# Kernel tuning notes

Measured on AMD Instinct MI355X. Metric: run time of the kernel, lower is better.

Reference implementation:

```python
import jax, jax.numpy as jnp
import numpy as np

N_NODES = 100000
N_EDGES = 1600000
D_IN = 64
D_OUT = 64
BN_EPS = 1e-5


def setup_inputs() -> dict:
    key = jax.random.key(0)
    ks = jax.random.split(key, 8)
    x = jax.random.normal(ks[0], (N_NODES, D_IN), dtype=jnp.float32)
    edge_index = jax.random.randint(ks[1], (2, N_EDGES), 0, N_NODES, dtype=jnp.int64)
    s_e = 1.0 / np.sqrt(2 * D_IN)
    s_n = 1.0 / np.sqrt(D_IN + D_OUT)
    W_edge = jax.random.uniform(ks[2], (2 * D_IN, D_OUT), jnp.float32, -s_e, s_e)
    b_edge = jax.random.uniform(ks[3], (D_OUT,), jnp.float32, -s_e, s_e)
    W_node = jax.random.uniform(ks[4], (D_IN + D_OUT, D_OUT), jnp.float32, -s_n, s_n)
    b_node = jax.random.uniform(ks[5], (D_OUT,), jnp.float32, -s_n, s_n)
    prelu_a = jnp.asarray(0.25, dtype=jnp.float32)  # nn.PReLU default single slope
    bn_gamma = jnp.ones((D_OUT,), dtype=jnp.float32)
    bn_beta = jnp.zeros((D_OUT,), dtype=jnp.float32)
    return {"x": x, "edge_index": edge_index, "W_edge": W_edge, "b_edge": b_edge,
            "W_node": W_node, "b_node": b_node, "prelu_a": prelu_a,
            "bn_gamma": bn_gamma, "bn_beta": bn_beta}


def reference(x, edge_index, W_edge, b_edge, W_node, b_node, prelu_a, bn_gamma, bn_beta):
    src, dst = edge_index[0], edge_index[1]
    # edge model: message from concat(source, target) node features  [E, 2*D_IN]
    msg_in = jnp.concatenate([x[src], x[dst]], axis=-1)
    msg = msg_in @ W_edge + b_edge                              # [E, D_OUT]
    # scatter-sum aggregate messages at destination nodes       [N, D_OUT]
    agg = jax.ops.segment_sum(msg, dst, num_segments=N_NODES)
    # node model
    h = jnp.concatenate([x, agg], axis=-1) @ W_node + b_node    # [N, D_OUT]
    # PReLU (single shared slope)
    h = jnp.where(h >= 0, h, prelu_a * h)
    # BatchNorm over nodes (training-mode batch stats, biased variance)
    mean = jnp.mean(h, axis=0)
    var = jnp.mean(jnp.square(h - mean), axis=0)
    h = (h - mean) * jax.lax.rsqrt(var + BN_EPS) * bn_gamma + bn_beta
    return h
```

## Files before the change

kernel.cpp:

```cpp
#include <hip/hip_runtime.h>
#include <hip/hip_fp16.h>

typedef _Float16 f16x8 __attribute__((ext_vector_type(8)));
typedef _Float16 f16x4 __attribute__((ext_vector_type(4)));
typedef float f32x4 __attribute__((ext_vector_type(4)));
typedef float f32x2 __attribute__((ext_vector_type(2)));

#define NPB 256
#define FCHUNK 6144
#define MAXBK 512
#define SEGCAP 64
#define CAP8 6144

__global__ __launch_bounds__(1024) void k_prepfill(
    const float4* __restrict__ x4, __half2* __restrict__ xh2,
    unsigned* __restrict__ xq, int n4, int X2,
    const int* __restrict__ src, const int* __restrict__ dst,
    int* __restrict__ cnt, int* __restrict__ packed2, int E, int FGRID,
    const float* __restrict__ We, const float* __restrict__ be,
    const float* __restrict__ Wn, __half* __restrict__ Wfrag, float* __restrict__ c2,
    float* __restrict__ stats, int nbuck, int N) {
  int b = blockIdx.x, t = threadIdx.x;
  if (b < X2) {
    int i = b * 1024 + t;
    if (i < n4) {
      float4 v = x4[i];
      __half2 a, c;
      a.x = __float2half_rn(v.x); a.y = __float2half_rn(v.y);
      c.x = __float2half_rn(v.z); c.y = __float2half_rn(v.w);
      xh2[2 * i] = a;
      xh2[2 * i + 1] = c;
      int w = __builtin_amdgcn_cvt_pk_fp8_f32(v.x, v.y, 0, false);
      w = __builtin_amdgcn_cvt_pk_fp8_f32(v.z, v.w, w, true);
      xq[i] = (unsigned)w;
    }
  } else if (b < X2 + 24) {
    int mb = b - X2;
    if (t < 512) {
      int mat = mb >> 3, kk = (mb >> 2) & 1, ct = mb & 3;
      int lane = t >> 3, j = t & 7;
      int k = kk * 32 + ((lane >> 4) & 3) * 8 + j;
      int col = ct * 16 + (lane & 15);
      float v;
      if (mat == 0) {
        v = Wn[k * 64 + col];
      } else if (mat == 1) {
        float a = 0.f;
        for (int m = 0; m < 64; ++m) a += We[k * 64 + m] * Wn[(64 + m) * 64 + col];
        v = a;
      } else {
        float a = 0.f;
        for (int m = 0; m < 64; ++m) a += We[(64 + k) * 64 + m] * Wn[(64 + m) * 64 + col];
        v = a;
      }
      Wfrag[mb * 512 + t] = __float2half_rn(v);
    }
  } else if (b == X2 + 24) {
    if (t < 64) {
      float a = 0.f;
      for (int m = 0; m < 64; ++m) a += be[m] * Wn[(64 + m) * 64 + t];
      c2[t] = a;
    } else if (t < 96) {
      __half2 z; z.x = __float2half_rn(0.f); z.y = __float2half_rn(0.f);
      xh2[(size_t)N * 32 + (t - 64)] = z;
    } else if (t < 112) {
      xq[(size_t)N * 16 + (t - 96)] = 0u;
    } else if (t >= 128 && t < 256) {
      stats[t - 128] = 0.f;
    }
  } else {
    int fb = b - (X2 + 25);
    __shared__ int lh[MAXBK];
    int e0 = fb * FCHUNK;
    int e1 = min(e0 + FCHUNK, E);
    for (int i = t; i < MAXBK; i += 1024) lh[i] = 0;
    __syncthreads();
    int dv[6];
#pragma unroll
    for (int i = 0; i < 6; ++i) {
      int e = e0 + t + i * 1024;
      dv[i] = (e < e1) ? dst[e] : -1;
      if (dv[i] >= 0) atomicAdd(&lh[dv[i] >> 8], 1);
    }
    __syncthreads();
    for (int i = t; i < MAXBK; i += 1024) {
      if (i < nbuck) cnt[(size_t)i * FGRID + fb] = lh[i];
      lh[i] = 0;
    }
    __syncthreads();
#pragma unroll
    for (int i = 0; i < 6; ++i) {
      int d = dv[i];
      if (d >= 0) {
        int e = e0 + t + i * 1024;
        int bk = d >> 8;
        unsigned lp = (unsigned)atomicAdd(&lh[bk], 1);
        if (lp < SEGCAP)
          packed2[((size_t)bk * FGRID + fb) * SEGCAP + lp] = src[e] | ((d & 255) << 20);
      }
    }
  }
}

__global__ __launch_bounds__(1024) void k_sort(const int* __restrict__ packed2,
    const int* __restrict__ cnt, int* __restrict__ csr,
    int* __restrict__ offA, int* __restrict__ deg, int FGRID, int N) {
  __shared__ int scnt[288];
  __shared__ int hist[NPB];
  __shared__ int sc[NPB];
  __shared__ int curs[NPB];
  int b = blockIdx.x, t = threadIdx.x;
  if (t < NPB) hist[t] = 0;
  for (int i = t; i < FGRID; i += 1024) scnt[i] = cnt[(size_t)b * FGRID + i];
  __syncthreads();
  int slots = FGRID * SEGCAP;
  const int* seg = packed2 + (size_t)b * FGRID * SEGCAP;
  for (int idx = t; idx < slots; idx += 1024) {
    int s = idx >> 6, k = idx & 63;
    if (k < scnt[s]) atomicAdd(&hist[(seg[idx] >> 20) & 255], 1);
  }
  __syncthreads();
  int v = (t < NPB) ? hist[t] : 0;
  int pv = (v + 7) & ~7;
  if (t < NPB) sc[t] = pv;
  __syncthreads();
  for (int d = 1; d < 256; d <<= 1) {
    int a = (t >= d && t < NPB) ? sc[t - d] : 0;
    __syncthreads();
    if (t < NPB) sc[t] += a;
    __syncthreads();
  }
  if (t < NPB) {
    int ex = b * CAP8 + sc[t] - pv;
    curs[t] = ex;
    int n = b * NPB + t;
    if (n < N) { offA[n] = ex; deg[n] = v; }
    for (int k = v; k < pv; ++k) csr[ex + k] = N;
  }
  __syncthreads();
  for (int idx = t; idx < slots; idx += 1024) {
    int s = idx >> 6, k = idx & 63;
    if (k < scnt[s]) {
      int pk = seg[idx];
      int p = atomicAdd(&curs[(pk >> 20) & 255], 1);
      csr[p] = pk & 0xFFFFF;
    }
  }
}

#define FBATCH8(J0, J, AL, AH)                                                 \
  {                                                                            \
    int u_ = __builtin_amdgcn_readfirstlane((J0) + (J));                       \
    int e0_ = csr[u_ + 0], e1_ = csr[u_ + 1], e2_ = csr[u_ + 2], e3_ = csr[u_ + 3]; \
    int e4_ = csr[u_ + 4], e5_ = csr[u_ + 5], e6_ = csr[u_ + 6], e7_ = csr[u_ + 7]; \
    int p1_ = (slot & 1) ? e1_ : e0_, q1_ = (slot & 1) ? e3_ : e2_;            \
    int s1_ = (slot & 2) ? q1_ : p1_;                                          \
    int p2_ = (slot & 1) ? e5_ : e4_, q2_ = (slot & 1) ? e7_ : e6_;            \
    int s2_ = (slot & 2) ? q2_ : p2_;                                          \
    unsigned w1_ = xq[((unsigned)s1_ << 4) | q];                               \
    unsigned w2_ = xq[((unsigned)s2_ << 4) | q];                               \
    f32x2 l1_ = __builtin_amdgcn_cvt_pk_f32_fp8(w1_, false);                   \
    f32x2 h1_ = __builtin_amdgcn_cvt_pk_f32_fp8(w1_, true);                    \
    f32x2 l2_ = __builtin_amdgcn_cvt_pk_f32_fp8(w2_, false);                   \
    f32x2 h2_ = __builtin_amdgcn_cvt_pk_f32_fp8(w2_, true);                    \
    AL += l1_; AH += h1_; AL += l2_; AH += h2_;                                \
  }

__global__ void k_agg(const unsigned* __restrict__ xq, const int* __restrict__ offA,
                      const int* __restrict__ deg, const int* __restrict__ csr,
                      __half* __restrict__ Sh, int N) {
  int t = threadIdx.x;
  unsigned lane = t & 63;
  unsigned q = lane & 15;
  int slot = (int)(lane >> 4);
  int wid = (blockIdx.x * blockDim.x + t) >> 6;
  int nw = (gridDim.x * blockDim.x) >> 6;
  for (int n = wid; n < N; n += 2 * nw) {
    int nB = n + nw;
    int j0A = offA[n];
    int pdA = (deg[n] + 7) & ~7;
    int j0B = (nB < N) ? offA[nB] : 0;
    int pdB = (nB < N) ? ((deg[nB] + 7) & ~7) : 0;
    f32x2 aAL = {0.f, 0.f}, aAH = {0.f, 0.f};
    f32x2 aBL = {0.f, 0.f}, aBH = {0.f, 0.f};
    int jA = 0, jB = 0;
    for (; jA < pdA && jB < pdB; jA += 8, jB += 8) {
      FBATCH8(j0A, jA, aAL, aAH)
      FBATCH8(j0B, jB, aBL, aBH)
    }
    for (; jA < pdA; jA += 8) FBATCH8(j0A, jA, aAL, aAH)
    for (; jB < pdB; jB += 8) FBATCH8(j0B, jB, aBL, aBH)
    aAL.x += __shfl_xor(aAL.x, 16); aAL.y += __shfl_xor(aAL.y, 16);
    aAH.x += __shfl_xor(aAH.x, 16); aAH.y += __shfl_xor(aAH.y, 16);
    aAL.x += __shfl_xor(aAL.x, 32); aAL.y += __shfl_xor(aAL.y, 32);
    aAH.x += __shfl_xor(aAH.x, 32); aAH.y += __shfl_xor(aAH.y, 32);
    if (slot == 0) {
      f16x4 o;
      o[0] = (_Float16)aAL.x; o[1] = (_Float16)aAL.y;
      o[2] = (_Float16)aAH.x; o[3] = (_Float16)aAH.y;
      *(f16x4*)(Sh + ((size_t)n << 6) + (q << 2)) = o;
    }
    if (nB < N) {
      aBL.x += __shfl_xor(aBL.x, 16); aBL.y += __shfl_xor(aBL.y, 16);
      aBH.x += __shfl_xor(aBH.x, 16); aBH.y += __shfl_xor(aBH.y, 16);
      aBL.x += __shfl_xor(aBL.x, 32); aBL.y += __shfl_xor(aBL.y, 32);
      aBH.x += __shfl_xor(aBH.x, 32); aBH.y += __shfl_xor(aBH.y, 32);
      if (slot == 0) {
        f16x4 o;
        o[0] = (_Float16)aBL.x; o[1] = (_Float16)aBL.y;
        o[2] = (_Float16)aBH.x; o[3] = (_Float16)aBH.y;
        *(f16x4*)(Sh + ((size_t)nB << 6) + (q << 2)) = o;
      }
    }
  }
}

__global__ __launch_bounds__(256) void k_nodeM(const __half* __restrict__ xh,
    const __half* __restrict__ Sh, const int* __restrict__ deg,
    const __half* __restrict__ Wfrag, const float* __restrict__ c2,
    const float* __restrict__ bnode, const float* __restrict__ pa,
    __half* __restrict__ Hh, float* __restrict__ pstats, int N) {
  __shared__ float ls[128];
  const f16x8* WF = (const f16x8*)Wfrag;
  int t = threadIdx.x, lane = t & 63;
  if (t < 128) ls[t] = 0.f;
  f16x8 B[24];
#pragma unroll
  for (int f = 0; f < 24; ++f) B[f] = WF[f * 64 + lane];
  float slope = pa[0];
  int wid = (blockIdx.x * blockDim.x + t) >> 6;
  int nw = (gridDim.x * blockDim.x) >> 6;
  int ntile = N >> 4;
  int r = lane & 15, g = lane >> 4;
  float ws[4] = {0, 0, 0, 0}, wq[4] = {0, 0, 0, 0};
  __syncthreads();
  for (int tile = wid; tile < ntile; tile += nw) {
    int n0 = tile << 4;
    float dg[4];
#pragma unroll
    for (int qq = 0; qq < 4; ++qq) dg[qq] = (float)deg[n0 + g * 4 + qq];
    const f16x8* xp = (const f16x8*)(xh + (size_t)(n0 + r) * 64 + g * 8);
    const f16x8* sp = (const f16x8*)(Sh + (size_t)(n0 + r) * 64 + g * 8);
    f16x8 ax0 = xp[0], ax1 = xp[4];
    f16x8 as0 = sp[0], as1 = sp[4];
    f32x4 accA[4], accB[4];
#pragma unroll
    for (int ct = 0; ct < 4; ++ct) {
      f32x4 a = {0.f, 0.f, 0.f, 0.f};
      a = __builtin_amdgcn_mfma_f32_16x16x32_f16(ax0, B[0 + ct], a, 0, 0, 0);
      a = __builtin_amdgcn_mfma_f32_16x16x32_f16(ax1, B[4 + ct], a, 0, 0, 0);
      a = __builtin_amdgcn_mfma_f32_16x16x32_f16(as0, B[8 + ct], a, 0, 0, 0);
      a = __builtin_amdgcn_mfma_f32_16x16x32_f16(as1, B[12 + ct], a, 0, 0, 0);
      accA[ct] = a;
      f32x4 bb = {0.f, 0.f, 0.f, 0.f};
      bb = __builtin_amdgcn_mfma_f32_16x16x32_f16(ax0, B[16 + ct], bb, 0, 0, 0);
      bb = __builtin_amdgcn_mfma_f32_16x16x32_f16(ax1, B[20 + ct], bb, 0, 0, 0);
      accB[ct] = bb;
    }
#pragma unroll
    for (int ct = 0; ct < 4; ++ct) {
      int c = ct * 16 + r;
      float cc = c2[c], bv = bnode[c];
#pragma unroll
      for (int qq = 0; qq < 4; ++qq) {
        float hv = accA[ct][qq] + dg[qq] * (accB[ct][qq] + cc) + bv;
        hv = hv >= 0.f ? hv : slope * hv;
        ws[ct] += hv; wq[ct] += hv * hv;
        Hh[(size_t)(n0 + g * 4 + qq) * 64 + c] = __float2half_rn(hv);
      }
    }
  }
#pragma unroll
  for (int ct = 0; ct < 4; ++ct) {
    int c = ct * 16 + r;
    atomicAdd(&ls[c], ws[ct]);
    atomicAdd(&ls[64 + c], wq[ct]);
  }
  __syncthreads();
  if (t < 128) pstats[(size_t)blockIdx.x * 128 + t] = ls[t];
}

__global__ __launch_bounds__(256) void k_stats(const float* __restrict__ pstats,
    float* __restrict__ stats, int nb) {
  int t = threadIdx.x;
  int col = t & 127;
  int half = t >> 7;
  float acc = 0.f;
  for (int i = blockIdx.x * 2 + half; i < nb; i += gridDim.x * 2)
    acc += pstats[(size_t)i * 128 + col];
  atomicAdd(&stats[col], acc);
}

__global__ void k_out2(const __half2* __restrict__ hh, const float* __restrict__ stats,
                       const float* __restrict__ gamma, const float* __restrict__ beta,
                       float2* __restrict__ out2, int n2, float invN) {
  int i = blockIdx.x * blockDim.x + threadIdx.x;
  if (i < n2) {
    int cb = (i & 31) * 2;
    float m0 = stats[cb] * invN, m1 = stats[cb + 1] * invN;
    float v0 = stats[64 + cb] * invN - m0 * m0;
    float v1 = stats[64 + cb + 1] * invN - m1 * m1;
    float sc0 = gamma[cb] * rsqrtf(v0 + 1e-5f);
    float sc1 = gamma[cb + 1] * rsqrtf(v1 + 1e-5f);
    float sh0 = beta[cb] - m0 * sc0;
    float sh1 = beta[cb + 1] - m1 * sc1;
    __half2 v = hh[i];
    float2 o;
    o.x = __half2float(v.x) * sc0 + sh0;
    o.y = __half2float(v.y) * sc1 + sh1;
    out2[i] = o;
  }
}


extern "C" void kernel_launch(void* const* d_in, const int* in_sizes, int n_in,
                              void* d_out, int out_size, void* d_ws, size_t ws_size,
                              hipStream_t stream) {
  const float* x     = (const float*)d_in[0];
  const int*   ei    = (const int*)d_in[1];
  const float* We    = (const float*)d_in[2];
  const float* be    = (const float*)d_in[3];
  const float* Wn    = (const float*)d_in[4];
  const float* bnode = (const float*)d_in[5];
  const float* pa    = (const float*)d_in[6];
  const float* gamma = (const float*)d_in[7];
  const float* beta  = (const float*)d_in[8];

  int N = in_sizes[0] / 64;
  int E = in_sizes[1] / 2;
  const int* srcA = ei;
  const int* dstA = ei + E;

  int NBUCK = (N + NPB - 1) / NPB;
  int FGRID = (E + FCHUNK - 1) / FCHUNK;

  char* ws = (char*)d_ws;
  size_t off = 0;
  auto alloc = [&](size_t bytes) -> void* {
    void* p = (void*)(ws + off);
    off += (bytes + 255) & ~(size_t)255;
    return p;
  };
  int ntile = N / 16;
  int mgrid = (ntile + 3) / 4;

  float*    stats   = (float*)alloc(128 * 4);
  int*      cnt     = (int*)alloc((size_t)NBUCK * FGRID * 4);
  int*      packed2 = (int*)alloc((size_t)NBUCK * FGRID * SEGCAP * 4);
  int*      csr     = (int*)alloc((size_t)NBUCK * CAP8 * 4);
  int*      offA    = (int*)alloc((size_t)N * 4);
  int*      deg     = (int*)alloc((size_t)N * 4);
  __half*   xh      = (__half*)alloc((size_t)(N + 1) * 64 * 2);
  unsigned* xq      = (unsigned*)alloc((size_t)(N + 1) * 64);
  __half*   Sh      = (__half*)alloc((size_t)N * 64 * 2);
  __half*   Hh      = (__half*)alloc((size_t)N * 64 * 2);
  __half*   Wfrag   = (__half*)alloc((size_t)24 * 512 * 2);
  float*    c2      = (float*)alloc(64 * 4);
  float*    pstats  = (float*)alloc((size_t)mgrid * 128 * 4);

  int n4 = N * 16;
  int X2 = (n4 + 1023) / 1024;
  int n2 = N * 32;
  int pgrid = X2 + 25 + FGRID;

  k_prepfill<<<pgrid, 1024, 0, stream>>>(
      (const float4*)x, (__half2*)xh, xq, n4, X2,
      srcA, dstA, cnt, packed2, E, FGRID,
      We, be, Wn, Wfrag, c2, stats, NBUCK, N);
  k_sort<<<NBUCK, 1024, 0, stream>>>(packed2, cnt, csr, offA, deg, FGRID, N);
  k_agg<<<2048, 256, 0, stream>>>(xq, offA, deg, csr, Sh, N);
  k_nodeM<<<mgrid, 256, 0, stream>>>(xh, Sh, deg, Wfrag, c2, bnode, pa, Hh, pstats, N);
  k_stats<<<64, 256, 0, stream>>>(pstats, stats, mgrid);
  k_out2<<<(n2 + 255) / 256, 256, 0, stream>>>((const __half2*)Hh, stats, gamma, beta,
                                               (float2*)d_out, n2, 1.0f / (float)N);
}
```

Baseline: 119.3 us.

## Fuse bucket sort and aggregation, keeping per-bucket CSR in shared memory

Merges the sort and aggregate kernels so each block builds its bucket's CSR in LDS and then aggregates its 128 nodes directly from it. Bucket size is halved to 128 nodes and the segment capacity to 32, which shrinks the packed staging buffer. This removes the global CSR, offA writes and reads, and one kernel launch. In exchange, parallelism in aggregation drops to 8 waves per bucket with a fixed node assignment, and overflow risk rises with the smaller SEGCAP and CAPL caps.

```diff
diff --git a/kernel.cpp b/kernel.cpp
--- a/kernel.cpp
+++ b/kernel.cpp
@@ -6,11 +6,10 @@
 typedef float f32x4 __attribute__((ext_vector_type(4)));
 typedef float f32x2 __attribute__((ext_vector_type(2)));
 
-#define NPB 256
+#define NPB 128
 #define FCHUNK 6144
-#define MAXBK 512
-#define SEGCAP 64
-#define CAP8 6144
+#define SEGCAP 32
+#define CAPL 3584
 
 __global__ __launch_bounds__(1024) void k_prepfill(
     const float4* __restrict__ x4, __half2* __restrict__ xh2,
@@ -70,89 +69,41 @@
     }
   } else {
     int fb = b - (X2 + 25);
-    __shared__ int lh[MAXBK];
+    __shared__ int lh[1024];
     int e0 = fb * FCHUNK;
     int e1 = min(e0 + FCHUNK, E);
-    for (int i = t; i < MAXBK; i += 1024) lh[i] = 0;
+    lh[t] = 0;
     __syncthreads();
     int dv[6];
 #pragma unroll
     for (int i = 0; i < 6; ++i) {
       int e = e0 + t + i * 1024;
       dv[i] = (e < e1) ? dst[e] : -1;
-      if (dv[i] >= 0) atomicAdd(&lh[dv[i] >> 8], 1);
-    }
-    __syncthreads();
-    for (int i = t; i < MAXBK; i += 1024) {
-      if (i < nbuck) cnt[(size_t)i * FGRID + fb] = lh[i];
-      lh[i] = 0;
-    }
+      if (dv[i] >= 0) atomicAdd(&lh[dv[i] >> 7], 1);
+    }
+    __syncthreads();
+    if (t < nbuck) cnt[(size_t)t * FGRID + fb] = lh[t];
+    lh[t] = 0;
     __syncthreads();
 #pragma unroll
     for (int i = 0; i < 6; ++i) {
       int d = dv[i];
       if (d >= 0) {
         int e = e0 + t + i * 1024;
-        int bk = d >> 8;
+        int bk = d >> 7;
         unsigned lp = (unsigned)atomicAdd(&lh[bk], 1);
         if (lp < SEGCAP)
-          packed2[((size_t)bk * FGRID + fb) * SEGCAP + lp] = src[e] | ((d & 255) << 20);
-      }
-    }
-  }
-}
-
-__global__ __launch_bounds__(1024) void k_sort(const int* __restrict__ packed2,
-    const int* __restrict__ cnt, int* __restrict__ csr,
-    int* __restrict__ offA, int* __restrict__ deg, int FGRID, int N) {
-  __shared__ int scnt[288];
-  __shared__ int hist[NPB];
-  __shared__ int sc[NPB];
-  __shared__ int curs[NPB];
-  int b = blockIdx.x, t = threadIdx.x;
-  if (t < NPB) hist[t] = 0;
-  for (int i = t; i < FGRID; i += 1024) scnt[i] = cnt[(size_t)b * FGRID + i];
-  __syncthreads();
-  int slots = FGRID * SEGCAP;
-  const int* seg = packed2 + (size_t)b * FGRID * SEGCAP;
-  for (int idx = t; idx < slots; idx += 1024) {
-    int s = idx >> 6, k = idx & 63;
-    if (k < scnt[s]) atomicAdd(&hist[(seg[idx] >> 20) & 255], 1);
-  }
-  __syncthreads();
-  int v = (t < NPB) ? hist[t] : 0;
-  int pv = (v + 7) & ~7;
-  if (t < NPB) sc[t] = pv;
-  __syncthreads();
-  for (int d = 1; d < 256; d <<= 1) {
-    int a = (t >= d && t < NPB) ? sc[t - d] : 0;
-    __syncthreads();
-    if (t < NPB) sc[t] += a;
-    __syncthreads();
-  }
-  if (t < NPB) {
-    int ex = b * CAP8 + sc[t] - pv;
-    curs[t] = ex;
-    int n = b * NPB + t;
-    if (n < N) { offA[n] = ex; deg[n] = v; }
-    for (int k = v; k < pv; ++k) csr[ex + k] = N;
-  }
-  __syncthreads();
-  for (int idx = t; idx < slots; idx += 1024) {
-    int s = idx >> 6, k = idx & 63;
-    if (k < scnt[s]) {
-      int pk = seg[idx];
-      int p = atomicAdd(&curs[(pk >> 20) & 255], 1);
-      csr[p] = pk & 0xFFFFF;
-    }
-  }
-}
-
-#define FBATCH8(J0, J, AL, AH)                                                 \
+          packed2[((size_t)bk * FGRID + fb) * SEGCAP + lp] = src[e] | ((d & 127) << 20);
+      }
+    }
+  }
+}
+
+#define LBATCH8(J0, J, AL, AH)                                                 \
   {                                                                            \
-    int u_ = __builtin_amdgcn_readfirstlane((J0) + (J));                       \
-    int e0_ = csr[u_ + 0], e1_ = csr[u_ + 1], e2_ = csr[u_ + 2], e3_ = csr[u_ + 3]; \
-    int e4_ = csr[u_ + 4], e5_ = csr[u_ + 5], e6_ = csr[u_ + 6], e7_ = csr[u_ + 7]; \
+    int u_ = (J0) + (J);                                                       \
+    int e0_ = csrL[u_ + 0], e1_ = csrL[u_ + 1], e2_ = csrL[u_ + 2], e3_ = csrL[u_ + 3]; \
+    int e4_ = csrL[u_ + 4], e5_ = csrL[u_ + 5], e6_ = csrL[u_ + 6], e7_ = csrL[u_ + 7]; \
     int p1_ = (slot & 1) ? e1_ : e0_, q1_ = (slot & 1) ? e3_ : e2_;            \
     int s1_ = (slot & 2) ? q1_ : p1_;                                          \
     int p2_ = (slot & 1) ? e5_ : e4_, q2_ = (slot & 1) ? e7_ : e6_;            \
@@ -166,50 +117,92 @@
     AL += l1_; AH += h1_; AL += l2_; AH += h2_;                                \
   }
 
-__global__ void k_agg(const unsigned* __restrict__ xq, const int* __restrict__ offA,
-                      const int* __restrict__ deg, const int* __restrict__ csr,
-                      __half* __restrict__ Sh, int N) {
-  int t = threadIdx.x;
+__global__ __launch_bounds__(512) void k_sortagg(
+    const int* __restrict__ packed2, const int* __restrict__ cnt,
+    const unsigned* __restrict__ xq, int* __restrict__ deg,
+    __half* __restrict__ Sh, int FGRID, int N) {
+  __shared__ int scnt[264];
+  __shared__ int hist[NPB];
+  __shared__ int sc[NPB];
+  __shared__ int curs[NPB];
+  __shared__ int csrL[CAPL];
+  int b = blockIdx.x, t = threadIdx.x;
+  if (t < NPB) hist[t] = 0;
+  for (int i = t; i < FGRID; i += 512) scnt[i] = cnt[(size_t)b * FGRID + i];
+  __syncthreads();
+  int slots = FGRID * SEGCAP;
+  const int* seg = packed2 + (size_t)b * FGRID * SEGCAP;
+  for (int idx = t; idx < slots; idx += 512) {
+    int s = idx >> 5, k = idx & 31;
+    if (k < scnt[s]) atomicAdd(&hist[(seg[idx] >> 20) & 127], 1);
+  }
+  __syncthreads();
+  int v = (t < NPB) ? hist[t] : 0;
+  int pv = (v + 7) & ~7;
+  if (t < NPB) sc[t] = pv;
+  __syncthreads();
+  for (int d = 1; d < NPB; d <<= 1) {
+    int a = (t >= d && t < NPB) ? sc[t - d] : 0;
+    __syncthreads();
+    if (t < NPB) sc[t] += a;
+    __syncthreads();
+  }
+  if (t < NPB) {
+    int ex = sc[t] - pv;
+    curs[t] = ex;
+    int n = b * NPB + t;
+    if (n < N) deg[n] = v;
+    for (int k = v; k < pv; ++k) csrL[ex + k] = N;
+  }
+  __syncthreads();
+  for (int idx = t; idx < slots; idx += 512) {
+    int s = idx >> 5, k = idx & 31;
+    if (k < scnt[s]) {
+      int pk = seg[idx];
+      int p = atomicAdd(&curs[(pk >> 20) & 127], 1);
+      csrL[p] = pk & 0xFFFFF;
+    }
+  }
+  __syncthreads();
+  int w = t >> 6;
   unsigned lane = t & 63;
   unsigned q = lane & 15;
   int slot = (int)(lane >> 4);
-  int wid = (blockIdx.x * blockDim.x + t) >> 6;
-  int nw = (gridDim.x * blockDim.x) >> 6;
-  for (int n = wid; n < N; n += 2 * nw) {
-    int nB = n + nw;
-    int j0A = offA[n];
-    int pdA = (deg[n] + 7) & ~7;
-    int j0B = (nB < N) ? offA[nB] : 0;
-    int pdB = (nB < N) ? ((deg[nB] + 7) & ~7) : 0;
+  for (int p = 0; p < 16; p += 2) {
+    int ln = w * 16 + p;
+    int vA = hist[ln], vB = hist[ln + 1];
+    int pdA = (vA + 7) & ~7, pdB = (vB + 7) & ~7;
+    int j0A = sc[ln] - pdA, j0B = sc[ln + 1] - pdB;
     f32x2 aAL = {0.f, 0.f}, aAH = {0.f, 0.f};
     f32x2 aBL = {0.f, 0.f}, aBH = {0.f, 0.f};
     int jA = 0, jB = 0;
     for (; jA < pdA && jB < pdB; jA += 8, jB += 8) {
-      FBATCH8(j0A, jA, aAL, aAH)
-      FBATCH8(j0B, jB, aBL, aBH)
-    }
-    for (; jA < pdA; jA += 8) FBATCH8(j0A, jA, aAL, aAH)
-    for (; jB < pdB; jB += 8) FBATCH8(j0B, jB, aBL, aBH)
+      LBATCH8(j0A, jA, aAL, aAH)
+      LBATCH8(j0B, jB, aBL, aBH)
+    }
+    for (; jA < pdA; jA += 8) LBATCH8(j0A, jA, aAL, aAH)
+    for (; jB < pdB; jB += 8) LBATCH8(j0B, jB, aBL, aBH)
     aAL.x += __shfl_xor(aAL.x, 16); aAL.y += __shfl_xor(aAL.y, 16);
     aAH.x += __shfl_xor(aAH.x, 16); aAH.y += __shfl_xor(aAH.y, 16);
     aAL.x += __shfl_xor(aAL.x, 32); aAL.y += __shfl_xor(aAL.y, 32);
     aAH.x += __shfl_xor(aAH.x, 32); aAH.y += __shfl_xor(aAH.y, 32);
+    aBL.x += __shfl_xor(aBL.x, 16); aBL.y += __shfl_xor(aBL.y, 16);
+    aBH.x += __shfl_xor(aBH.x, 16); aBH.y += __shfl_xor(aBH.y, 16);
+    aBL.x += __shfl_xor(aBL.x, 32); aBL.y += __shfl_xor(aBL.y, 32);
+    aBH.x += __shfl_xor(aBH.x, 32); aBH.y += __shfl_xor(aBH.y, 32);
+    int n = b * NPB + ln;
     if (slot == 0) {
-      f16x4 o;
-      o[0] = (_Float16)aAL.x; o[1] = (_Float16)aAL.y;
-      o[2] = (_Float16)aAH.x; o[3] = (_Float16)aAH.y;
-      *(f16x4*)(Sh + ((size_t)n << 6) + (q << 2)) = o;
-    }
-    if (nB < N) {
-      aBL.x += __shfl_xor(aBL.x, 16); aBL.y += __shfl_xor(aBL.y, 16);
-      aBH.x += __shfl_xor(aBH.x, 16); aBH.y += __shfl_xor(aBH.y, 16);
-      aBL.x += __shfl_xor(aBL.x, 32); aBL.y += __shfl_xor(aBL.y, 32);
-      aBH.x += __shfl_xor(aBH.x, 32); aBH.y += __shfl_xor(aBH.y, 32);
-      if (slot == 0) {
+      if (n < N) {
+        f16x4 o;
+        o[0] = (_Float16)aAL.x; o[1] = (_Float16)aAL.y;
+        o[2] = (_Float16)aAH.x; o[3] = (_Float16)aAH.y;
+        *(f16x4*)(Sh + ((size_t)n << 6) + (q << 2)) = o;
+      }
+      if (n + 1 < N) {
         f16x4 o;
         o[0] = (_Float16)aBL.x; o[1] = (_Float16)aBL.y;
         o[2] = (_Float16)aBH.x; o[3] = (_Float16)aBH.y;
-        *(f16x4*)(Sh + ((size_t)nB << 6) + (q << 2)) = o;
+        *(f16x4*)(Sh + ((size_t)(n + 1) << 6) + (q << 2)) = o;
       }
     }
   }
@@ -347,8 +340,6 @@
   float*    stats   = (float*)alloc(128 * 4);
   int*      cnt     = (int*)alloc((size_t)NBUCK * FGRID * 4);
   int*      packed2 = (int*)alloc((size_t)NBUCK * FGRID * SEGCAP * 4);
-  int*      csr     = (int*)alloc((size_t)NBUCK * CAP8 * 4);
-  int*      offA    = (int*)alloc((size_t)N * 4);
   int*      deg     = (int*)alloc((size_t)N * 4);
   __half*   xh      = (__half*)alloc((size_t)(N + 1) * 64 * 2);
   unsigned* xq      = (unsigned*)alloc((size_t)(N + 1) * 64);
@@ -367,8 +358,7 @@
       (const float4*)x, (__half2*)xh, xq, n4, X2,
       srcA, dstA, cnt, packed2, E, FGRID,
       We, be, Wn, Wfrag, c2, stats, NBUCK, N);
-  k_sort<<<NBUCK, 1024, 0, stream>>>(packed2, cnt, csr, offA, deg, FGRID, N);
-  k_agg<<<2048, 256, 0, stream>>>(xq, offA, deg, csr, Sh, N);
+  k_sortagg<<<NBUCK, 512, 0, stream>>>(packed2, cnt, xq, deg, Sh, FGRID, N);
   k_nodeM<<<mgrid, 256, 0, stream>>>(xh, Sh, deg, Wfrag, c2, bnode, pa, Hh, pstats, N);
   k_stats<<<64, 256, 0, stream>>>(pstats, stats, mgrid);
   k_out2<<<(n2 + 255) / 256, 256, 0, stream>>>((const __half2*)Hh, stats, gamma, beta,
```

Measured after the change: 115.3 us. -3.3%, faster.
